# Kernel optimization log

Hardware: AMD Instinct MI355X
Metric: run time of the kernel (lower is better)

Reference implementation:

```python
import jax, jax.numpy as jnp
import numpy as np

D_MODEL = 512
D_STATE = 16
EPS = 1e-8
LN_EPS = 1e-5


def setup_inputs() -> dict:
    key = jax.random.key(0)
    ks = jax.random.split(key, 9)
    B, N = 4, 2048
    x = jax.random.normal(ks[0], (B, N, D_MODEL), dtype=jnp.float32)
    A_log = jax.random.normal(ks[1], (D_STATE,), dtype=jnp.float32) * 0.1 - 1.0
    # xavier_uniform with gain=0.5 for B and C linear weights
    lim_B = 0.5 * np.sqrt(6.0 / (D_MODEL + D_STATE))
    W_B = jax.random.uniform(ks[2], (D_STATE, D_MODEL), jnp.float32, -lim_B, lim_B)
    W_C = jax.random.uniform(ks[3], (D_MODEL, D_STATE), jnp.float32, -lim_B, lim_B)
    D = jax.random.normal(ks[4], (D_MODEL,), dtype=jnp.float32) * 0.01
    lim_g = np.sqrt(1.0 / D_MODEL)  # torch Linear default init
    W_gate = jax.random.uniform(ks[5], (D_MODEL, D_MODEL), jnp.float32, -lim_g, lim_g)
    b_gate = jax.random.uniform(ks[6], (D_MODEL,), jnp.float32, -lim_g, lim_g)
    ln_gamma = jnp.ones((D_MODEL,), jnp.float32)
    ln_beta = jnp.zeros((D_MODEL,), jnp.float32)
    return {"x": x, "A_log": A_log, "W_B": W_B, "W_C": W_C, "D": D,
            "W_gate": W_gate, "b_gate": b_gate, "ln_gamma": ln_gamma, "ln_beta": ln_beta}


def reference(x, A_log, W_B, W_C, D, W_gate, b_gate, ln_gamma, ln_beta):
    Bb, N, Dm = x.shape
    A = -jnp.clip(jnp.exp(A_log), EPS, 10.0)                      # (d_state,)
    dt = 1.0 / N
    A_bar = jnp.exp(dt * A)                                       # (d_state,)
    B_bar = jnp.where(jnp.abs(A) > EPS, (A_bar - 1.0) / (A + EPS),
                      jnp.full_like(A, dt))
    Bu = jnp.einsum('bnm,sm->bns', x, W_B) * B_bar                # (B,N,d_state)
    idx = jnp.arange(N)
    diff = jnp.clip(idx[None, :] - idx[:, None], 0, None)[..., None]  # (N,N,1)
    decay = A_bar[None, None, :] ** diff                          # (N,N,d_state)
    mask = (idx[None, :] >= idx[:, None])[..., None]
    decay = decay * mask.astype(decay.dtype)
    h = jnp.einsum('nms,bns->bms', decay, Bu)                     # (B,N,d_state)
    h = jnp.clip(h, -10.0, 10.0)
    y = jnp.einsum('bns,ms->bnm', h, W_C) + D * x                 # (B,N,d_model)
    gate = jax.nn.sigmoid(jnp.einsum('bnm,km->bnk', x, W_gate) + b_gate)
    y = gate * y + (1.0 - gate) * x
    # LayerNorm (dropout is identity in eval mode)
    mu = jnp.mean(y, axis=-1, keepdims=True)
    var = jnp.var(y, axis=-1, keepdims=True)
    return (y - mu) / jnp.sqrt(var + LN_EPS) * ln_gamma + ln_beta
```

## Files before the change

### kernel.cpp

```cpp
#include <hip/hip_runtime.h>
#include <math.h>
#include <stdint.h>

#define D_MODEL 512
#define D_STATE 16
#define NSEQ    2048
#define NBATCH  4
#define EPSF    1e-8f
#define LN_EPSF 1e-5f
#define DT      (1.0f / 2048.0f)

typedef __attribute__((ext_vector_type(8))) short short8;
typedef __attribute__((ext_vector_type(4))) float floatx4;

__device__ __forceinline__ ushort f2bf(float f) {
    uint32_t u = __float_as_uint(f);
    return (ushort)((u + 0x7fffu + ((u >> 16) & 1u)) >> 16);
}

__global__ __launch_bounds__(256) void kP(const float* __restrict__ x,
                                          const float* __restrict__ A_log,
                                          const float* __restrict__ W_B,
                                          const float* __restrict__ Wg,
                                          ushort* __restrict__ wgb,
                                          float* __restrict__ hL,
                                          float* __restrict__ states) {
    __shared__ float wb[D_STATE][D_MODEL + 4];
    __shared__ float bbars[16], abars[16];
    __shared__ float w4[4][16];
    const int tid = threadIdx.x, lane = tid & 63, wave = tid >> 6;

    if (tid < 64) {
        int i = blockIdx.x * 64 + tid;
        const float4* sp = (const float4*)Wg + (size_t)i * 2;
        float4 a = sp[0], b = sp[1];
        float v[8] = {a.x, a.y, a.z, a.w, b.x, b.y, b.z, b.w};
        short8 o;
        #pragma unroll
        for (int j = 0; j < 8; ++j) o[j] = (short)f2bf(v[j]);
        *(short8*)(wgb + (size_t)i * 8) = o;
    }
    if (tid < 16) {
        float A    = -fminf(fmaxf(expf(A_log[tid]), EPSF), 10.0f);
        float Abar = expf(A * DT);
        abars[tid] = Abar;
        bbars[tid] = (fabsf(A) > EPSF) ? (Abar - 1.0f) / (A + EPSF) : DT;
    }
    __syncthreads();
    for (int i = tid; i < D_STATE * D_MODEL; i += 256) {
        int s = i >> 9, m = i & 511;
        wb[s][m] = W_B[i] * bbars[s];
    }
    __syncthreads();

    const int s    = lane & 15;
    const int q    = lane >> 4;
    const int rloc = q + (wave << 2);
    const int row  = blockIdx.x * 16 + rloc;
    const float* xr = x + (size_t)row * D_MODEL;

    float acc = 0.f;
    #pragma unroll 4
    for (int m = 0; m < D_MODEL; m += 4) {
        float4 xv = *(const float4*)(xr + m);
        float4 wv = *(const float4*)(&wb[s][m]);
        acc += xv.x * wv.x + xv.y * wv.y + xv.z * wv.z + xv.w * wv.w;
    }

    float abar = abars[s];
    float a = abar, b = acc;
    {
        float ap = __shfl_up(a, 16), bp = __shfl_up(b, 16);
        if (lane >= 16) { b = a * bp + b; a = a * ap; }
    }
    {
        float ap = __shfl_up(a, 32), bp = __shfl_up(b, 32);
        if (lane >= 32) { b = a * bp + b; a = a * ap; }
    }
    if (q == 3) w4[wave][s] = b;
    __syncthreads();
    float a4 = abar * abar; a4 = a4 * a4;
    float pb = 0.f;
    for (int w = 0; w < wave; ++w) pb = a4 * pb + w4[w][s];
    float hloc = a * pb + b;

    hL[(size_t)row * D_STATE + s] = hloc;
    if (rloc == 15) states[(size_t)blockIdx.x * D_STATE + s] = hloc;
}

#define CBM 16
#define BKC 32
__global__ __launch_bounds__(256) void kc_fused(
    const float*  __restrict__ x,
    const ushort* __restrict__ Wg,
    const float*  __restrict__ hL,
    const float*  __restrict__ states,
    const float*  __restrict__ A_log,
    const float*  __restrict__ W_C,
    const float*  __restrict__ Dvec,
    const float*  __restrict__ bg,
    const float*  __restrict__ gamma,
    const float*  __restrict__ beta,
    float* __restrict__ out) {
    __shared__ ushort Bsub[512 * BKC];
    __shared__ ushort wcs[512 * 16];
    __shared__ ushort Asub[CBM * BKC];
    __shared__ ushort hs[CBM * 16];
    __shared__ float  red[4][CBM][2];

    const int tid  = threadIdx.x;
    const int lane = tid & 63, wave = tid >> 6;
    const int r0   = blockIdx.x * CBM;
    const int fr   = lane & 15, kg = lane >> 4;
    const int colw = wave * 128;

    float* stg = (float*)Bsub;
    const int c0 = blockIdx.x & 127;
    for (int i = tid; i < c0 * 16; i += 256)
        stg[i] = states[(size_t)(blockIdx.x - c0) * 16 + i];

    #pragma unroll
    for (int it = 0; it < 4; ++it) {
        int idx = it * 256 + tid;
        int row = idx >> 1, g = idx & 1;
        const float4* src = (const float4*)(W_C + (size_t)row * D_STATE + g * 8);
        float4 v0 = src[0], v1 = src[1];
        float v[8] = {v0.x,v0.y,v0.z,v0.w,v1.x,v1.y,v1.z,v1.w};
        short8 o;
        #pragma unroll
        for (int e = 0; e < 8; ++e) o[e] = (short)f2bf(v[e]);
        *(short8*)(wcs + row * 16 + (g ^ (row & 1)) * 8) = o;
    }
    __syncthreads();

    {
        int s = tid & 15, nloc = tid >> 4;
        float A   = -fminf(fmaxf(expf(A_log[s]), EPSF), 10.0f);
        float a16 = expf(A * DT * 16.0f);
        float p = 0.f;
        for (int cc = 0; cc < c0; ++cc) p = a16 * p + stg[cc * 16 + s];
        float hv = expf(A * DT * (float)(nloc + 1)) * p
                 + hL[(size_t)(r0 + nloc) * D_STATE + s];
        hv = fminf(fmaxf(hv, -10.f), 10.f);
        hs[nloc * 16 + (((s >> 3) ^ (nloc & 1)) * 8) + (s & 7)] = f2bf(hv);
    }

    floatx4 acc[8] = {};
    const int arow = tid >> 4;
    const int akp  = (tid & 15) * 2;

    for (int kc = 0; kc < D_MODEL; kc += BKC) {
        const float* axp = x + (size_t)(r0 + arow) * D_MODEL + kc + akp;
        float2 av = *(const float2*)axp;

        __syncthreads();

        {
            int g = akp >> 3;
            int addr = arow * BKC + ((g ^ (arow & 3)) * 8) + (akp & 7);
            ushort2 o; o.x = f2bf(av.x); o.y = f2bf(av.y);
            *(ushort2*)(Asub + addr) = o;
        }
        #pragma unroll
        for (int is = 0; is < 8; ++is) {
            int row = is * 64 + (tid >> 2);
            int g   = (tid & 3) ^ (row & 3);
            const ushort* gsrc = Wg + (size_t)row * D_MODEL + kc + g * 8;
            __builtin_amdgcn_global_load_lds(
                (const __attribute__((address_space(1))) void*)gsrc,
                (__attribute__((address_space(3))) void*)((char*)Bsub + is * 4096 + tid * 16),
                16, 0, 0);
        }
        __syncthreads();

        short8 af = *(const short8*)(Asub + fr * BKC + ((kg ^ (fr & 3)) * 8));
        #pragma unroll
        for (int j = 0; j < 8; ++j) {
            int rb = colw + j * 16 + fr;
            short8 bv = *(const short8*)(Bsub + (size_t)rb * BKC + ((kg ^ (rb & 3)) * 8));
            acc[j] = __builtin_amdgcn_mfma_f32_16x16x32_bf16(af, bv, acc[j], 0, 0, 0);
        }
    }

    const short8 z8 = short8{0,0,0,0,0,0,0,0};
    short8 ah = (kg < 2) ? *(const short8*)(hs + fr * 16 + ((kg ^ (fr & 1)) * 8)) : z8;
    floatx4 yc[8] = {};
    #pragma unroll
    for (int j = 0; j < 8; ++j) {
        int rb = colw + j * 16 + fr;
        short8 bw = (kg < 2) ? *(const short8*)(wcs + rb * 16 + ((kg ^ (rb & 1)) * 8)) : z8;
        yc[j] = __builtin_amdgcn_mfma_f32_16x16x32_bf16(ah, bw, yc[j], 0, 0, 0);
    }

    float vsum[4] = {}, vsq[4] = {};
    #pragma unroll
    for (int j = 0; j < 8; ++j) {
        int col = colw + j * 16 + fr;
        float dv = Dvec[col], bgv = bg[col];
        #pragma unroll
        for (int q = 0; q < 4; ++q) {
            int rl = kg * 4 + q;
            float xv = x[(size_t)(r0 + rl) * D_MODEL + col];
            float lg = acc[j][q] + bgv;
            float gt = 1.f / (1.f + expf(-lg));
            float yv = yc[j][q] + dv * xv;
            float v  = gt * yv + (1.f - gt) * xv;
            acc[j][q] = v;
            vsum[q] += v;
            vsq[q]  += v * v;
        }
    }
    #pragma unroll
    for (int off = 1; off < 16; off <<= 1) {
        #pragma unroll
        for (int q = 0; q < 4; ++q) {
            vsum[q] += __shfl_xor(vsum[q], off);
            vsq[q]  += __shfl_xor(vsq[q], off);
        }
    }
    if (fr == 0) {
        #pragma unroll
        for (int q = 0; q < 4; ++q) {
            red[wave][kg * 4 + q][0] = vsum[q];
            red[wave][kg * 4 + q][1] = vsq[q];
        }
    }
    __syncthreads();
    float mu[4], rs[4];
    #pragma unroll
    for (int q = 0; q < 4; ++q) {
        int rl = kg * 4 + q;
        float s = 0.f, ss = 0.f;
        #pragma unroll
        for (int w = 0; w < 4; ++w) { s += red[w][rl][0]; ss += red[w][rl][1]; }
        float m   = s * (1.f / (float)D_MODEL);
        float var = ss * (1.f / (float)D_MODEL) - m * m;
        mu[q] = m;
        rs[q] = rsqrtf(var + LN_EPSF);
    }
    #pragma unroll
    for (int j = 0; j < 8; ++j) {
        int col = colw + j * 16 + fr;
        float ga = gamma[col], be = beta[col];
        #pragma unroll
        for (int q = 0; q < 4; ++q)
            out[(size_t)(r0 + kg * 4 + q) * D_MODEL + col] =
                (acc[j][q] - mu[q]) * rs[q] * ga + be;
    }
}

extern "C" void kernel_launch(void* const* d_in, const int* in_sizes, int n_in,
                              void* d_out, int out_size, void* d_ws, size_t ws_size,
                              hipStream_t stream) {
    const float* x     = (const float*)d_in[0];
    const float* A_log = (const float*)d_in[1];
    const float* W_B   = (const float*)d_in[2];
    const float* W_C   = (const float*)d_in[3];
    const float* Dv    = (const float*)d_in[4];
    const float* Wg    = (const float*)d_in[5];
    const float* bg    = (const float*)d_in[6];
    const float* gamma = (const float*)d_in[7];
    const float* beta  = (const float*)d_in[8];
    float* out = (float*)d_out;

    const int rows = NBATCH * NSEQ;

    ushort* wgb    = (ushort*)d_ws;
    float*  hL     = (float*)(wgb + (size_t)D_MODEL * D_MODEL);
    float*  states = hL + (size_t)rows * D_STATE;

    hipLaunchKernelGGL(kP, dim3(rows / 16), dim3(256), 0, stream,
                       x, A_log, W_B, Wg, wgb, hL, states);
    hipLaunchKernelGGL(kc_fused, dim3(rows / CBM), dim3(256), 0, stream,
                       x, wgb, hL, states, A_log, W_C, Dv, bg, gamma, beta, out);
}
```

Measured before the change: 47.01 us.

## Double-buffer gate weight tiles and compute SSM output projection in fp32 directly

```diff
diff --git a/kernel.cpp b/kernel.cpp
--- a/kernel.cpp
+++ b/kernel.cpp
@@ -102,10 +102,8 @@
     const float*  __restrict__ gamma,
     const float*  __restrict__ beta,
     float* __restrict__ out) {
-    __shared__ ushort Bsub[512 * BKC];
-    __shared__ ushort wcs[512 * 16];
-    __shared__ ushort Asub[CBM * BKC];
-    __shared__ ushort hs[CBM * 16];
+    __shared__ ushort Bsub[2][512 * BKC];
+    __shared__ float  hsf[CBM][D_STATE];
     __shared__ float  red[4][CBM][2];
 
     const int tid  = threadIdx.x;
@@ -114,25 +112,11 @@
     const int fr   = lane & 15, kg = lane >> 4;
     const int colw = wave * 128;
 
-    float* stg = (float*)Bsub;
+    float* stg = (float*)Bsub[1];
     const int c0 = blockIdx.x & 127;
     for (int i = tid; i < c0 * 16; i += 256)
         stg[i] = states[(size_t)(blockIdx.x - c0) * 16 + i];
-
-    #pragma unroll
-    for (int it = 0; it < 4; ++it) {
-        int idx = it * 256 + tid;
-        int row = idx >> 1, g = idx & 1;
-        const float4* src = (const float4*)(W_C + (size_t)row * D_STATE + g * 8);
-        float4 v0 = src[0], v1 = src[1];
-        float v[8] = {v0.x,v0.y,v0.z,v0.w,v1.x,v1.y,v1.z,v1.w};
-        short8 o;
-        #pragma unroll
-        for (int e = 0; e < 8; ++e) o[e] = (short)f2bf(v[e]);
-        *(short8*)(wcs + row * 16 + (g ^ (row & 1)) * 8) = o;
-    }
-    __syncthreads();
-
+    __syncthreads();
     {
         int s = tid & 15, nloc = tid >> 4;
         float A   = -fminf(fmaxf(expf(A_log[s]), EPSF), 10.0f);
@@ -141,55 +125,57 @@
         for (int cc = 0; cc < c0; ++cc) p = a16 * p + stg[cc * 16 + s];
         float hv = expf(A * DT * (float)(nloc + 1)) * p
                  + hL[(size_t)(r0 + nloc) * D_STATE + s];
-        hv = fminf(fmaxf(hv, -10.f), 10.f);
-        hs[nloc * 16 + (((s >> 3) ^ (nloc & 1)) * 8) + (s & 7)] = f2bf(hv);
-    }
+        hsf[nloc][s] = fminf(fmaxf(hv, -10.f), 10.f);
+    }
+    __syncthreads();
+
+    const int srow = tid >> 2;
+    const int sp   = tid & 3;
+
+    #define STAGE_B(bb, kcc)                                                      \
+      { _Pragma("unroll")                                                         \
+        for (int is = 0; is < 8; ++is) {                                          \
+          int row_ = is * 64 + srow;                                              \
+          int g_   = sp ^ (row_ & 3);                                             \
+          const ushort* gsrc_ = Wg + (size_t)row_ * D_MODEL + (kcc) + g_ * 8;     \
+          __builtin_amdgcn_global_load_lds(                                       \
+            (const __attribute__((address_space(1))) void*)gsrc_,                 \
+            (__attribute__((address_space(3))) void*)((char*)Bsub[bb] + is * 4096 + tid * 16), \
+            16, 0, 0);                                                            \
+        } }
+
+    const float* aptr = x + (size_t)(r0 + fr) * D_MODEL + kg * 8;
+    float4 av0 = *(const float4*)aptr;
+    float4 av1 = *(const float4*)(aptr + 4);
+    STAGE_B(0, 0);
+    __syncthreads();
 
     floatx4 acc[8] = {};
-    const int arow = tid >> 4;
-    const int akp  = (tid & 15) * 2;
-
-    for (int kc = 0; kc < D_MODEL; kc += BKC) {
-        const float* axp = x + (size_t)(r0 + arow) * D_MODEL + kc + akp;
-        float2 av = *(const float2*)axp;
-
-        __syncthreads();
-
+    int buf = 0;
+    for (int t = 0; t < 16; ++t) {
+        const int kc = t * BKC;
+        float4 nv0 = av0, nv1 = av1;
+        if (t < 15) {
+            const float* ap = x + (size_t)(r0 + fr) * D_MODEL + kc + BKC + kg * 8;
+            nv0 = *(const float4*)ap;
+            nv1 = *(const float4*)(ap + 4);
+            STAGE_B(buf ^ 1, kc + BKC);
+        }
+        short8 af;
         {
-            int g = akp >> 3;
-            int addr = arow * BKC + ((g ^ (arow & 3)) * 8) + (akp & 7);
-            ushort2 o; o.x = f2bf(av.x); o.y = f2bf(av.y);
-            *(ushort2*)(Asub + addr) = o;
-        }
-        #pragma unroll
-        for (int is = 0; is < 8; ++is) {
-            int row = is * 64 + (tid >> 2);
-            int g   = (tid & 3) ^ (row & 3);
-            const ushort* gsrc = Wg + (size_t)row * D_MODEL + kc + g * 8;
-            __builtin_amdgcn_global_load_lds(
-                (const __attribute__((address_space(1))) void*)gsrc,
-                (__attribute__((address_space(3))) void*)((char*)Bsub + is * 4096 + tid * 16),
-                16, 0, 0);
-        }
-        __syncthreads();
-
-        short8 af = *(const short8*)(Asub + fr * BKC + ((kg ^ (fr & 3)) * 8));
+            float v[8] = {av0.x,av0.y,av0.z,av0.w,av1.x,av1.y,av1.z,av1.w};
+            #pragma unroll
+            for (int e = 0; e < 8; ++e) af[e] = (short)f2bf(v[e]);
+        }
         #pragma unroll
         for (int j = 0; j < 8; ++j) {
             int rb = colw + j * 16 + fr;
-            short8 bv = *(const short8*)(Bsub + (size_t)rb * BKC + ((kg ^ (rb & 3)) * 8));
+            short8 bv = *(const short8*)(&Bsub[buf][(size_t)rb * BKC + ((kg ^ (rb & 3)) * 8)]);
             acc[j] = __builtin_amdgcn_mfma_f32_16x16x32_bf16(af, bv, acc[j], 0, 0, 0);
         }
-    }
-
-    const short8 z8 = short8{0,0,0,0,0,0,0,0};
-    short8 ah = (kg < 2) ? *(const short8*)(hs + fr * 16 + ((kg ^ (fr & 1)) * 8)) : z8;
-    floatx4 yc[8] = {};
-    #pragma unroll
-    for (int j = 0; j < 8; ++j) {
-        int rb = colw + j * 16 + fr;
-        short8 bw = (kg < 2) ? *(const short8*)(wcs + rb * 16 + ((kg ^ (rb & 1)) * 8)) : z8;
-        yc[j] = __builtin_amdgcn_mfma_f32_16x16x32_bf16(ah, bw, yc[j], 0, 0, 0);
+        __syncthreads();
+        av0 = nv0; av1 = nv1;
+        buf ^= 1;
     }
 
     float vsum[4] = {}, vsq[4] = {};
@@ -197,13 +183,20 @@
     for (int j = 0; j < 8; ++j) {
         int col = colw + j * 16 + fr;
         float dv = Dvec[col], bgv = bg[col];
+        const float4* wcp = (const float4*)(W_C + (size_t)col * D_STATE);
+        float4 w0 = wcp[0], w1 = wcp[1], w2 = wcp[2], w3 = wcp[3];
         #pragma unroll
         for (int q = 0; q < 4; ++q) {
             int rl = kg * 4 + q;
             float xv = x[(size_t)(r0 + rl) * D_MODEL + col];
+            const float* hp = hsf[rl];
+            float yv = dv * xv
+                + hp[0]*w0.x + hp[1]*w0.y + hp[2]*w0.z + hp[3]*w0.w
+                + hp[4]*w1.x + hp[5]*w1.y + hp[6]*w1.z + hp[7]*w1.w
+                + hp[8]*w2.x + hp[9]*w2.y + hp[10]*w2.z + hp[11]*w2.w
+                + hp[12]*w3.x + hp[13]*w3.y + hp[14]*w3.z + hp[15]*w3.w;
             float lg = acc[j][q] + bgv;
             float gt = 1.f / (1.f + expf(-lg));
-            float yv = yc[j][q] + dv * xv;
             float v  = gt * yv + (1.f - gt) * xv;
             acc[j][q] = v;
             vsum[q] += v;
```

Measured after the change: 64.39 us. 37.0% more time.
